# Kernel tuning notes

Measured on AMD Instinct MI355X. Metric: run time of the kernel, lower is better.

The kernel has to match this reference:

```python
import math
import jax, jax.numpy as jnp
import numpy as np


def positional_encoding(c, h, w):
    # Faithful port of the torch positional_encode grid (c divisible by 4).
    half = c // 2
    div = jnp.exp(jnp.arange(0, half, 2, dtype=jnp.float32) * (-math.log(10000.0) / half))  # [half/2]
    pos_w = jnp.arange(w, dtype=jnp.float32)[:, None]  # [w,1]
    pos_h = jnp.arange(h, dtype=jnp.float32)[:, None]  # [h,1]
    q = half // 2
    pe = jnp.zeros((c, h, w), dtype=jnp.float32)
    sw = jnp.sin(pos_w * div).T[:, None, :]  # [q,1,w] -> broadcast over height
    cw = jnp.cos(pos_w * div).T[:, None, :]
    sh = jnp.sin(pos_h * div).T[:, :, None]  # [q,h,1] -> broadcast over width
    ch = jnp.cos(pos_h * div).T[:, :, None]
    pe = pe.at[0:half:2].set(jnp.broadcast_to(sw, (q, h, w)))
    pe = pe.at[1:half:2].set(jnp.broadcast_to(cw, (q, h, w)))
    pe = pe.at[half::2].set(jnp.broadcast_to(sh, (q, h, w)))
    pe = pe.at[half + 1::2].set(jnp.broadcast_to(ch, (q, h, w)))
    return pe


def setup_inputs() -> dict:
    key = jax.random.key(0)
    k1, k2, k3, k4 = jax.random.split(key, 4)
    b, c, h, w = 4, 256, 64, 64
    x = jax.random.normal(k1, (b, c, h, w), dtype=jnp.float32)
    # kaiming_uniform-ish scale for d x d weights
    bound = 1.0 / math.sqrt(c)
    Wq = jax.random.uniform(k2, (c, c), dtype=jnp.float32, minval=-bound, maxval=bound)
    Wk = jax.random.uniform(k3, (c, c), dtype=jnp.float32, minval=-bound, maxval=bound)
    Wv = jax.random.uniform(k4, (c, c), dtype=jnp.float32, minval=-bound, maxval=bound)
    return {"x": x, "Wq": Wq, "Wk": Wk, "Wv": Wv}


def reference(x, Wq, Wk, Wv):
    b, c, h, w = x.shape
    pe = positional_encoding(c, h, w)
    xt = (x + pe).reshape(b, c, h * w).transpose(0, 2, 1)  # [b, hw, c]
    Q = xt @ Wq  # [b, hw, c]
    K = xt @ Wk
    V = xt @ Wv
    scores = jnp.einsum('bqc,bkc->bqk', Q, K) / math.sqrt(c)  # [b, hw, hw]
    # NOTE: softmax over dim=1 (the QUERY axis), matching nn.Softmax(dim=1)
    A = jax.nn.softmax(scores, axis=1)
    out = jnp.einsum('bqk,bkc->bqc', A, V)  # [b, hw, c]
    return out.transpose(0, 2, 1).reshape(b, c, h, w)
```

## Files before the change

### kernel.cpp

```cpp
#include <hip/hip_runtime.h>
#include <hip/hip_bf16.h>
#include <math.h>

typedef float f32x4 __attribute__((ext_vector_type(4)));
typedef short bf16x8 __attribute__((ext_vector_type(8)));
typedef short bf16x4 __attribute__((ext_vector_type(4)));

#define AS1 __attribute__((address_space(1)))
#define AS3 __attribute__((address_space(3)))

__device__ __forceinline__ short f2bf(float f) {
    unsigned u = __float_as_uint(f);
    unsigned r = (u + 0x7fffu + ((u >> 16) & 1u)) >> 16;
    return (short)r;
}
__device__ __forceinline__ float bf2f(short s) {
    return __uint_as_float(((unsigned)(unsigned short)s) << 16);
}
__device__ __forceinline__ void gld16(const void* g, void* l) {
    __builtin_amdgcn_global_load_lds((const AS1 unsigned int*)g, (AS3 unsigned int*)l, 16, 0, 0);
}

__device__ __forceinline__ void stage128x64(const short* __restrict__ g,
                                            short* lds, int t) {
    int w = t >> 6, l = t & 63;
    #pragma unroll
    for (int j = 0; j < 4; ++j) {
        int ii = j * 4 + w;
        int row = ii * 8 + (l >> 3);
        int slot = (l & 7) ^ (row & 7);
        gld16(g + row * 256 + slot * 8, lds + ii * 512);
    }
}

__global__ __launch_bounds__(256) void k_prep(const float* __restrict__ x,
                                              const float* __restrict__ Wq,
                                              const float* __restrict__ Wk,
                                              const float* __restrict__ Wv,
                                              short* __restrict__ xt,
                                              short* __restrict__ Wt) {
    int bidx = blockIdx.x;
    if (bidx < 768) {
        int wsel = bidx >> 8, n = bidx & 255, k = threadIdx.x;
        const float* W = (wsel == 0) ? Wq : (wsel == 1) ? Wk : Wv;
        Wt[(wsel * 256 + n) * 256 + k] = f2bf(W[k * 256 + n]);
        return;
    }
    int bid = bidx - 768;
    int b = bid >> 7;
    int pb = bid & 127;
    __shared__ __align__(16) float tile[256][33];
    __shared__ __align__(16) float pew[128][32];
    __shared__ __align__(16) float peh[128];
    int t = threadIdx.x;
    const float c1 = 0.14391156f;
    int wbase = (pb & 1) * 32;
    int hpos = pb >> 1;
    #pragma unroll
    for (int j = 0; j < 16; ++j) {
        int idx = t + j * 256;
        int c = idx >> 5, pp = idx & 31;
        int i = c >> 1;
        float d = expf(-(float)i * c1);
        float arg = (float)(wbase + pp) * d;
        pew[c][pp] = (c & 1) ? cosf(arg) : sinf(arg);
    }
    if (t < 128) {
        int i = t >> 1;
        float d = expf(-(float)i * c1);
        float arg = (float)hpos * d;
        peh[t] = (t & 1) ? cosf(arg) : sinf(arg);
    }
    int p0 = pb * 32;
    #pragma unroll
    for (int j = 0; j < 32; ++j) {
        int c = j * 8 + (t >> 5);
        int pp = t & 31;
        tile[c][pp] = x[((b * 256 + c) << 12) + p0 + pp];
    }
    __syncthreads();
    int pp = t >> 3, cseg = t & 7;
    int p = p0 + pp;
    short* dst = xt + (((b << 12) + p) << 8) + (cseg << 5);
    #pragma unroll
    for (int j = 0; j < 4; ++j) {
        bf16x8 v;
        #pragma unroll
        for (int e = 0; e < 8; ++e) {
            int c = cseg * 32 + j * 8 + e;
            float pe = (c < 128) ? pew[c][pp] : peh[c - 128];
            v[e] = f2bf(tile[c][pp] + pe);
        }
        ((bf16x8*)dst)[j] = v;
    }
}

__global__ __launch_bounds__(256, 4) void k_proj(const short* __restrict__ xt,
                                                 const short* __restrict__ Wt,
                                                 short* __restrict__ Q,
                                                 short* __restrict__ K,
                                                 short* __restrict__ VT) {
    int id = blockIdx.x;
    int wsel = id % 3; id /= 3;
    int nt = id & 1;  id >>= 1;
    int mt = id & 31; int b = id >> 5;
    int t = threadIdx.x, l = t & 63, w = t >> 6;
    int lr = l & 15, lg = l >> 4;
    int wr = w >> 1, wc = w & 1;
    __shared__ __align__(16) short Xa[128 * 64];
    __shared__ __align__(16) short Wa[128 * 64];
    const short* Xg = xt + (((size_t)b << 12) + mt * 128) * 256;
    const short* Wg = Wt + ((size_t)wsel * 256 + nt * 128) * 256;
    f32x4 acc[4][4] = {};

    #pragma unroll
    for (int ks = 0; ks < 4; ++ks) {
        stage128x64(Xg + ks * 64, Xa, t);
        stage128x64(Wg + ks * 64, Wa, t);
        __syncthreads();
        #pragma unroll
        for (int s = 0; s < 2; ++s) {
            bf16x8 af[4], bw[4];
            #pragma unroll
            for (int ms = 0; ms < 4; ++ms) {
                int row = wr * 64 + ms * 16 + lr;
                af[ms] = *(const bf16x8*)(Xa + row * 64 + (((s * 4 + lg) ^ (row & 7)) << 3));
            }
            #pragma unroll
            for (int fn = 0; fn < 4; ++fn) {
                int row = wc * 64 + fn * 16 + lr;
                bw[fn] = *(const bf16x8*)(Wa + row * 64 + (((s * 4 + lg) ^ (row & 7)) << 3));
            }
            #pragma unroll
            for (int ms = 0; ms < 4; ++ms)
                #pragma unroll
                for (int fn = 0; fn < 4; ++fn)
                    acc[ms][fn] = __builtin_amdgcn_mfma_f32_16x16x32_bf16(af[ms], bw[fn], acc[ms][fn], 0, 0, 0);
        }
        __syncthreads();
    }

    int m0 = mt * 128 + wr * 64;
    int n0 = nt * 128 + wc * 64;
    if (wsel < 2) {
        float scl = (wsel == 0) ? 0.0625f : 1.0f;
        short* dst = (wsel == 0) ? Q : K;
        #pragma unroll
        for (int ms = 0; ms < 4; ++ms)
            #pragma unroll
            for (int fn = 0; fn < 4; ++fn)
                #pragma unroll
                for (int r = 0; r < 4; ++r) {
                    int m = m0 + ms * 16 + lg * 4 + r;
                    int n = n0 + fn * 16 + lr;
                    dst[((b << 12) + m) * 256 + n] = f2bf(acc[ms][fn][r] * scl);
                }
    } else {
        #pragma unroll
        for (int ms = 0; ms < 4; ++ms)
            #pragma unroll
            for (int fn = 0; fn < 4; ++fn) {
                int n = n0 + fn * 16 + lr;
                int m = m0 + ms * 16 + lg * 4;
                bf16x4 v;
                #pragma unroll
                for (int r = 0; r < 4; ++r) v[r] = f2bf(acc[ms][fn][r]);
                *(bf16x4*)(VT + ((b * 256 + n) << 12) + m) = v;
            }
    }
}

__global__ __launch_bounds__(512) void k_E(const short* __restrict__ Qm,
                                           const short* __restrict__ Km,
                                           short* __restrict__ E,
                                           float* __restrict__ pl) {
    int o = blockIdx.x;
    int bid = (o & 7) * 256 + (o >> 3);
    int qt = bid & 15, kt = (bid >> 4) & 31, b = bid >> 9;
    int t = threadIdx.x, l = t & 63;
    int w = t >> 6;
    int wrk = w & 1, wcq = w >> 1;
    int lr = l & 15, lg = l >> 4;
    __shared__ __align__(16) short Ka[128 * 64];
    __shared__ __align__(16) short Qa[256 * 64];
    __shared__ float plds[4 * 128];
    const short* Kg = Km + (((size_t)b << 12) + kt * 128) * 256;
    const short* Qg = Qm + (((size_t)b << 12) + qt * 256) * 256;
    f32x4 acc[4][4] = {};

    #pragma unroll
    for (int ks = 0; ks < 4; ++ks) {
        #pragma unroll
        for (int j = 0; j < 2; ++j) {
            int idx = j * 512 + t;
            int row = idx >> 3;
            int slot = (idx & 7) ^ (row & 7);
            gld16(Kg + ks * 64 + row * 256 + slot * 8, Ka + idx * 8);
        }
        #pragma unroll
        for (int j = 0; j < 4; ++j) {
            int idx = j * 512 + t;
            int row = idx >> 3;
            int slot = (idx & 7) ^ (row & 7);
            gld16(Qg + ks * 64 + row * 256 + slot * 8, Qa + idx * 8);
        }
        __syncthreads();
        #pragma unroll
        for (int s = 0; s < 2; ++s) {
            bf16x8 a[4], bq[4];
            #pragma unroll
            for (int mk = 0; mk < 4; ++mk) {
                int row = wrk * 64 + mk * 16 + lr;
                a[mk] = *(const bf16x8*)(Ka + row * 64 + (((s * 4 + lg) ^ (row & 7)) << 3));
            }
            #pragma unroll
            for (int nq = 0; nq < 4; ++nq) {
                int row = wcq * 64 + nq * 16 + lr;
                bq[nq] = *(const bf16x8*)(Qa + row * 64 + (((s * 4 + lg) ^ (row & 7)) << 3));
            }
            #pragma unroll
            for (int mk = 0; mk < 4; ++mk)
                #pragma unroll
                for (int nq = 0; nq < 4; ++nq)
                    acc[mk][nq] = __builtin_amdgcn_mfma_f32_16x16x32_bf16(a[mk], bq[nq], acc[mk][nq], 0, 0, 0);
        }
        __syncthreads();
    }

    int k0 = kt * 128 + wrk * 64;
    int q0 = qt * 256 + wcq * 64;
    float psum[4][4];
    #pragma unroll
    for (int mk = 0; mk < 4; ++mk) {
        float ps0 = 0.f, ps1 = 0.f, ps2 = 0.f, ps3 = 0.f;
        #pragma unroll
        for (int nq = 0; nq < 4; ++nq) {
            int q = q0 + nq * 16 + lr;
            float e0 = __expf(acc[mk][nq][0]);
            float e1 = __expf(acc[mk][nq][1]);
            float e2 = __expf(acc[mk][nq][2]);
            float e3 = __expf(acc[mk][nq][3]);
            ps0 += e0; ps1 += e1; ps2 += e2; ps3 += e3;
            bf16x4 ev;
            ev[0] = f2bf(e0); ev[1] = f2bf(e1); ev[2] = f2bf(e2); ev[3] = f2bf(e3);
            *(bf16x4*)(E + (((size_t)b << 12) + q) * 4096 + k0 + mk * 16 + lg * 4) = ev;
        }
        psum[mk][0] = ps0; psum[mk][1] = ps1; psum[mk][2] = ps2; psum[mk][3] = ps3;
    }
    #pragma unroll
    for (int mk = 0; mk < 4; ++mk)
        #pragma unroll
        for (int r = 0; r < 4; ++r) {
            float v = psum[mk][r];
            v += __shfl_xor(v, 1);
            v += __shfl_xor(v, 2);
            v += __shfl_xor(v, 4);
            v += __shfl_xor(v, 8);
            psum[mk][r] = v;
        }
    if (lr == 0) {
        #pragma unroll
        for (int mk = 0; mk < 4; ++mk)
            #pragma unroll
            for (int r = 0; r < 4; ++r)
                plds[wcq * 128 + wrk * 64 + mk * 16 + lg * 4 + r] = psum[mk][r];
    }
    __syncthreads();
    if (t < 128) {
        float s = plds[t] + plds[128 + t] + plds[256 + t] + plds[384 + t];
        pl[(b * 16 + qt) * 4096 + kt * 128 + t] = s;
    }
}

__global__ void k_lred(const float* __restrict__ pl, float* __restrict__ rl) {
    int gid = blockIdx.x * 256 + threadIdx.x;
    float s = 0.f;
    int b = gid >> 12, k = gid & 4095;
    #pragma unroll
    for (int qt = 0; qt < 16; ++qt) s += pl[(b * 16 + qt) * 4096 + k];
    rl[gid] = 1.0f / s;
}

__global__ void k_vn(const short* __restrict__ VT, const float* __restrict__ rl,
                     short* __restrict__ Vnt) {
    int gid = blockIdx.x * 256 + threadIdx.x;
    int idx8 = gid * 8;
    int b = idx8 >> 20;
    int rem = idx8 & 1048575;
    int k = rem & 4095;
    bf16x8 v = *(const bf16x8*)(VT + idx8);
    const float* rb = rl + (b << 12) + k;
    f32x4 r0 = *(const f32x4*)(rb);
    f32x4 r1 = *(const f32x4*)(rb + 4);
    bf16x8 oo;
    #pragma unroll
    for (int e = 0; e < 8; ++e) {
        float f = bf2f(v[e]);
        float rr = (e < 4) ? r0[e] : r1[e - 4];
        oo[e] = f2bf(f * rr);
    }
    *(bf16x8*)(Vnt + idx8) = oo;
}

__global__ __launch_bounds__(256) void k_pv(const short* __restrict__ E,
                                            const short* __restrict__ Vnt,
                                            float* __restrict__ out) {
    int o = blockIdx.x;
    int ct = o >> 8;
    int r = o & 255;
    int b = r >> 6, qt = r & 63;
    int t = threadIdx.x, l = t & 63, w = t >> 6;
    int wq = w >> 1, wc = w & 1;
    int lr = l & 15, lg = l >> 4;
    int q0 = qt * 64, c0 = ct * 128;
    __shared__ __align__(16) short Ea[64 * 128];
    __shared__ __align__(16) short Va[128 * 128];
    const short* Eg = E + (((size_t)b << 12) + q0) * 4096;
    const short* Vg = Vnt + ((size_t)(b * 256 + c0)) * 4096;
    f32x4 acc[2][4] = {};

    for (int kc = 0; kc < 4096; kc += 128) {
        #pragma unroll
        for (int j = 0; j < 4; ++j) {
            int idx = j * 256 + t;
            int row = idx >> 4;
            int slot = (idx & 15) ^ (row & 15);
            gld16(Eg + kc + (size_t)row * 4096 + slot * 8, Ea + idx * 8);
        }
        #pragma unroll
        for (int j = 0; j < 8; ++j) {
            int idx = j * 256 + t;
            int row = idx >> 4;
            int slot = (idx & 15) ^ (row & 15);
            gld16(Vg + kc + (size_t)row * 4096 + slot * 8, Va + idx * 8);
        }
        __syncthreads();
        #pragma unroll
        for (int s = 0; s < 4; ++s) {
            bf16x8 Af[2], Bf[4];
            #pragma unroll
            for (int mq = 0; mq < 2; ++mq) {
                int row = wq * 32 + mq * 16 + lr;
                Af[mq] = *(const bf16x8*)(Ea + row * 128 + (((s * 4 + lg) ^ (row & 15)) << 3));
            }
            #pragma unroll
            for (int nc = 0; nc < 4; ++nc) {
                int row = wc * 64 + nc * 16 + lr;
                Bf[nc] = *(const bf16x8*)(Va + row * 128 + (((s * 4 + lg) ^ (row & 15)) << 3));
            }
            #pragma unroll
            for (int mq = 0; mq < 2; ++mq)
                #pragma unroll
                for (int nc = 0; nc < 4; ++nc)
                    acc[mq][nc] = __builtin_amdgcn_mfma_f32_16x16x32_bf16(Af[mq], Bf[nc], acc[mq][nc], 0, 0, 0);
        }
        __syncthreads();
    }
    #pragma unroll
    for (int mq = 0; mq < 2; ++mq)
        #pragma unroll
        for (int nc = 0; nc < 4; ++nc) {
            int c = c0 + wc * 64 + nc * 16 + lr;
            int q = q0 + wq * 32 + mq * 16 + lg * 4;
            *(f32x4*)(out + (((size_t)b << 8) + c) * 4096 + q) = acc[mq][nc];
        }
}

extern "C" void kernel_launch(void* const* d_in, const int* in_sizes, int n_in,
                              void* d_out, int out_size, void* d_ws, size_t ws_size,
                              hipStream_t stream) {
    const float* x  = (const float*)d_in[0];
    const float* Wq = (const float*)d_in[1];
    const float* Wk = (const float*)d_in[2];
    const float* Wv = (const float*)d_in[3];

    char* p = (char*)d_ws;
    short* xt  = (short*)p; p += 4 * 4096 * 256 * 2;
    short* Wt  = (short*)p; p += 3 * 256 * 256 * 2;
    short* Qm  = (short*)p; p += 4 * 4096 * 256 * 2;
    short* Km  = (short*)p; p += 4 * 4096 * 256 * 2;
    short* VT  = (short*)p; p += 4 * 4096 * 256 * 2;
    short* E   = (short*)p; p += (size_t)4 * 4096 * 4096 * 2;
    float* pl  = (float*)p; p += 4 * 32 * 4096 * 4;
    float* rl  = (float*)p; p += 4 * 4096 * 4;
    short* Vnt = (short*)p; p += 4 * 4096 * 256 * 2;

    float* out = (float*)d_out;

    k_prep <<<1280, 256, 0, stream>>>(x, Wq, Wk, Wv, xt, Wt);
    k_proj <<<768, 256, 0, stream>>>(xt, Wt, Qm, Km, VT);
    k_E    <<<2048, 512, 0, stream>>>(Qm, Km, E, pl);
    k_lred <<<64,   256, 0, stream>>>(pl, rl);
    k_vn   <<<2048, 256, 0, stream>>>(VT, rl, Vnt);
    k_pv   <<<512,  256, 0, stream>>>(E, Vnt, out);
}
```

Baseline: 155.6 us.

## Store exp scores and normalized V in FP8 and use FP8 MFMA for PV

The unnormalized exp matrix E and the column-normalized V are now written as FP8 instead of bf16. The PV GEMM loads these bytes into LDS with a re-swizzled layout and uses the fp8 16x16x32 MFMA. V is pre-scaled by 4096 to stay in FP8 range, and the output is scaled back down. This halves the traffic of the large 4x4096x4096 E matrix on both the write and the read side. It trades that against reduced precision and a risk of accuracy-tolerance failures.

After: 145.5 us. -6.5%, faster.

```diff
diff --git a/kernel.cpp b/kernel.cpp
--- a/kernel.cpp
+++ b/kernel.cpp
@@ -172,7 +172,7 @@
 
 __global__ __launch_bounds__(512) void k_E(const short* __restrict__ Qm,
                                            const short* __restrict__ Km,
-                                           short* __restrict__ E,
+                                           unsigned char* __restrict__ E8,
                                            float* __restrict__ pl) {
     int o = blockIdx.x;
     int bid = (o & 7) * 256 + (o >> 3);
@@ -241,9 +241,10 @@
             float e2 = __expf(acc[mk][nq][2]);
             float e3 = __expf(acc[mk][nq][3]);
             ps0 += e0; ps1 += e1; ps2 += e2; ps3 += e3;
-            bf16x4 ev;
-            ev[0] = f2bf(e0); ev[1] = f2bf(e1); ev[2] = f2bf(e2); ev[3] = f2bf(e3);
-            *(bf16x4*)(E + (((size_t)b << 12) + q) * 4096 + k0 + mk * 16 + lg * 4) = ev;
+            int pk = 0;
+            pk = __builtin_amdgcn_cvt_pk_fp8_f32(e0, e1, pk, false);
+            pk = __builtin_amdgcn_cvt_pk_fp8_f32(e2, e3, pk, true);
+            *(unsigned*)(E8 + ((((size_t)b << 12) + q) * 4096) + k0 + mk * 16 + lg * 4) = (unsigned)pk;
         }
         psum[mk][0] = ps0; psum[mk][1] = ps1; psum[mk][2] = ps2; psum[mk][3] = ps3;
     }
@@ -282,28 +283,32 @@
 }
 
 __global__ void k_vn(const short* __restrict__ VT, const float* __restrict__ rl,
-                     short* __restrict__ Vnt) {
+                     unsigned char* __restrict__ Vn8) {
     int gid = blockIdx.x * 256 + threadIdx.x;
     int idx8 = gid * 8;
     int b = idx8 >> 20;
-    int rem = idx8 & 1048575;
-    int k = rem & 4095;
+    int k = idx8 & 4095;
     bf16x8 v = *(const bf16x8*)(VT + idx8);
     const float* rb = rl + (b << 12) + k;
     f32x4 r0 = *(const f32x4*)(rb);
     f32x4 r1 = *(const f32x4*)(rb + 4);
-    bf16x8 oo;
+    float f[8];
     #pragma unroll
     for (int e = 0; e < 8; ++e) {
-        float f = bf2f(v[e]);
         float rr = (e < 4) ? r0[e] : r1[e - 4];
-        oo[e] = f2bf(f * rr);
-    }
-    *(bf16x8*)(Vnt + idx8) = oo;
-}
-
-__global__ __launch_bounds__(256) void k_pv(const short* __restrict__ E,
-                                            const short* __restrict__ Vnt,
+        f[e] = bf2f(v[e]) * rr * 4096.0f;
+    }
+    int lo = 0, hi = 0;
+    lo = __builtin_amdgcn_cvt_pk_fp8_f32(f[0], f[1], lo, false);
+    lo = __builtin_amdgcn_cvt_pk_fp8_f32(f[2], f[3], lo, true);
+    hi = __builtin_amdgcn_cvt_pk_fp8_f32(f[4], f[5], hi, false);
+    hi = __builtin_amdgcn_cvt_pk_fp8_f32(f[6], f[7], hi, true);
+    uint2 u; u.x = (unsigned)lo; u.y = (unsigned)hi;
+    *(uint2*)(Vn8 + idx8) = u;
+}
+
+__global__ __launch_bounds__(256) void k_pv(const unsigned char* __restrict__ E8,
+                                            const unsigned char* __restrict__ Vn8,
                                             float* __restrict__ out) {
     int o = blockIdx.x;
     int ct = o >> 8;
@@ -313,46 +318,48 @@
     int wq = w >> 1, wc = w & 1;
     int lr = l & 15, lg = l >> 4;
     int q0 = qt * 64, c0 = ct * 128;
-    __shared__ __align__(16) short Ea[64 * 128];
-    __shared__ __align__(16) short Va[128 * 128];
-    const short* Eg = E + (((size_t)b << 12) + q0) * 4096;
-    const short* Vg = Vnt + ((size_t)(b * 256 + c0)) * 4096;
+    __shared__ __align__(16) unsigned char Ea8[64 * 128];
+    __shared__ __align__(16) unsigned char Va8[128 * 128];
+    const unsigned char* Eg = E8 + (((size_t)b << 12) + q0) * 4096;
+    const unsigned char* Vg = Vn8 + ((size_t)(b * 256 + c0)) * 4096;
     f32x4 acc[2][4] = {};
 
     for (int kc = 0; kc < 4096; kc += 128) {
+        #pragma unroll
+        for (int j = 0; j < 2; ++j) {
+            int idx = j * 256 + t;
+            int row = idx >> 3;
+            int slot = (idx & 7) ^ (row & 7);
+            gld16(Eg + kc + (size_t)row * 4096 + slot * 16, Ea8 + idx * 16);
+        }
         #pragma unroll
         for (int j = 0; j < 4; ++j) {
             int idx = j * 256 + t;
-            int row = idx >> 4;
-            int slot = (idx & 15) ^ (row & 15);
-            gld16(Eg + kc + (size_t)row * 4096 + slot * 8, Ea + idx * 8);
-        }
-        #pragma unroll
-        for (int j = 0; j < 8; ++j) {
-            int idx = j * 256 + t;
-            int row = idx >> 4;
-            int slot = (idx & 15) ^ (row & 15);
-            gld16(Vg + kc + (size_t)row * 4096 + slot * 8, Va + idx * 8);
+            int row = idx >> 3;
+            int slot = (idx & 7) ^ (row & 7);
+            gld16(Vg + kc + (size_t)row * 4096 + slot * 16, Va8 + idx * 16);
         }
         __syncthreads();
         #pragma unroll
         for (int s = 0; s < 4; ++s) {
-            bf16x8 Af[2], Bf[4];
+            int gchunk = s * 2 + (lg >> 1);
+            int off8 = (lg & 1) * 8;
+            long Af[2], Bf[4];
             #pragma unroll
             for (int mq = 0; mq < 2; ++mq) {
                 int row = wq * 32 + mq * 16 + lr;
-                Af[mq] = *(const bf16x8*)(Ea + row * 128 + (((s * 4 + lg) ^ (row & 15)) << 3));
+                Af[mq] = *(const long*)(Ea8 + row * 128 + ((gchunk ^ (row & 7)) << 4) + off8);
             }
             #pragma unroll
             for (int nc = 0; nc < 4; ++nc) {
                 int row = wc * 64 + nc * 16 + lr;
-                Bf[nc] = *(const bf16x8*)(Va + row * 128 + (((s * 4 + lg) ^ (row & 15)) << 3));
+                Bf[nc] = *(const long*)(Va8 + row * 128 + ((gchunk ^ (row & 7)) << 4) + off8);
             }
             #pragma unroll
             for (int mq = 0; mq < 2; ++mq)
                 #pragma unroll
                 for (int nc = 0; nc < 4; ++nc)
-                    acc[mq][nc] = __builtin_amdgcn_mfma_f32_16x16x32_bf16(Af[mq], Bf[nc], acc[mq][nc], 0, 0, 0);
+                    acc[mq][nc] = __builtin_amdgcn_mfma_f32_16x16x32_fp8_fp8(Af[mq], Bf[nc], acc[mq][nc], 0, 0, 0);
         }
         __syncthreads();
     }
@@ -362,7 +369,8 @@
         for (int nc = 0; nc < 4; ++nc) {
             int c = c0 + wc * 64 + nc * 16 + lr;
             int q = q0 + wq * 32 + mq * 16 + lg * 4;
-            *(f32x4*)(out + (((size_t)b << 8) + c) * 4096 + q) = acc[mq][nc];
+            f32x4 oo = acc[mq][nc] * 0.000244140625f;
+            *(f32x4*)(out + (((size_t)b << 8) + c) * 4096 + q) = oo;
         }
 }
 
@@ -380,17 +388,17 @@
     short* Qm  = (short*)p; p += 4 * 4096 * 256 * 2;
     short* Km  = (short*)p; p += 4 * 4096 * 256 * 2;
     short* VT  = (short*)p; p += 4 * 4096 * 256 * 2;
-    short* E   = (short*)p; p += (size_t)4 * 4096 * 4096 * 2;
+    unsigned char* E8 = (unsigned char*)p; p += (size_t)4 * 4096 * 4096 * 2;
     float* pl  = (float*)p; p += 4 * 32 * 4096 * 4;
     float* rl  = (float*)p; p += 4 * 4096 * 4;
-    short* Vnt = (short*)p; p += 4 * 4096 * 256 * 2;
+    unsigned char* Vn8 = (unsigned char*)p; p += 4 * 4096 * 256 * 2;
 
     float* out = (float*)d_out;
 
     k_prep <<<1280, 256, 0, stream>>>(x, Wq, Wk, Wv, xt, Wt);
     k_proj <<<768, 256, 0, stream>>>(xt, Wt, Qm, Km, VT);
-    k_E    <<<2048, 512, 0, stream>>>(Qm, Km, E, pl);
+    k_E    <<<2048, 512, 0, stream>>>(Qm, Km, E8, pl);
     k_lred <<<64,   256, 0, stream>>>(pl, rl);
-    k_vn   <<<2048, 256, 0, stream>>>(VT, rl, Vnt);
-    k_pv   <<<512,  256, 0, stream>>>(E, Vnt, out);
-}
+    k_vn   <<<2048, 256, 0, stream>>>(VT, rl, Vn8);
+    k_pv   <<<512,  256, 0, stream>>>(E8, Vn8, out);
+}
```
